# Performance work log

Measured on AMD Instinct MI355X. Metric: run time of the kernel, lower is better.

## Reference

```python
import jax, jax.numpy as jnp
import numpy as np

NUM_HEAD = 8
HIDDEN = 1024


def setup_inputs() -> dict:
    key = jax.random.key(0)
    ks = jax.random.split(key, 7)
    B, Q, K = 2, 256, 256
    return {
        "query": jax.random.normal(ks[0], (B, Q, HIDDEN), jnp.float32),
        "keys": jax.random.normal(ks[1], (B, K, HIDDEN), jnp.float32),
        "values": jax.random.normal(ks[2], (B, K, HIDDEN), jnp.float32),
        "mask": jax.random.randint(ks[3], (B, K), 0, 2, jnp.int32),
        "W_q": jax.random.normal(ks[4], (HIDDEN, HIDDEN), jnp.float32),
        "W_k": jax.random.normal(ks[5], (HIDDEN, HIDDEN), jnp.float32),
        "V_a": jax.random.normal(ks[6], (HIDDEN,), jnp.float32),
    }


def reference(query, keys, values, mask, W_q, W_k, V_a):
    B, Q, H = query.shape
    K = keys.shape[1]
    h_q = query @ W_q                                   # [B,Q,H]
    h_k = keys @ W_k                                    # [B,K,H]
    # additive (Bahdanau) scores, split hidden into heads and sum per head
    h = jnp.tanh(h_q[:, :, None, :] + h_k[:, None, :, :]) * V_a   # [B,Q,K,H]
    logits = h.reshape(B, Q, K, NUM_HEAD, H // NUM_HEAD).sum(-1)  # [B,Q,K,h]
    logits = jnp.transpose(logits, (0, 3, 1, 2))        # [B,h,Q,K]
    penalty = (1.0 - mask.astype(jnp.float32)) * 99.0   # [B,K]
    logits = logits - penalty[:, None, None, :]
    weights = jax.nn.softmax(logits, axis=-1)           # [B,h,Q,K]
    v = values.reshape(B, K, NUM_HEAD, H // NUM_HEAD)   # [B,K,h,d]
    ctx = jnp.einsum('bhqk,bkhd->bqhd', weights, v).reshape(B, Q, H)
    return ctx, weights
```

## Files before the change

### kernel.cpp

```cpp
#include <hip/hip_runtime.h>
#include <hip/hip_bf16.h>


#define TANH_SCALE 2.88539008177792681472f
#define LOG2E      1.44269504088896340736f

typedef __attribute__((ext_vector_type(8))) short bf16x8_t;
typedef __attribute__((ext_vector_type(4))) float f32x4_t;

__device__ inline ushort bf16_rne(float f) {
  unsigned u = __float_as_uint(f);
  u += 0x7FFFu + ((u >> 16) & 1u);
  return (ushort)(u >> 16);
}
__device__ inline float bf16_to_f(ushort h) { return __uint_as_float((unsigned)h << 16); }
__device__ inline void split1(float v, ushort& hi, ushort& lo) {
  hi = bf16_rne(v);
  lo = bf16_rne(v - bf16_to_f(hi));
}

__global__ __launch_bounds__(256) void prep(
    const float* __restrict__ query, const float* __restrict__ keys,
    const float* __restrict__ Wq, const float* __restrict__ Wk,
    ushort* __restrict__ qhi, ushort* __restrict__ qlo,
    ushort* __restrict__ khi, ushort* __restrict__ klo,
    ushort* __restrict__ wqthi, ushort* __restrict__ wqtlo,
    ushort* __restrict__ wkthi, ushort* __restrict__ wktlo)
{
  __shared__ float t[64][65];
  const int bid = blockIdx.x, tid = threadIdx.x;
  if (bid < 1024) {
    const int z = bid >> 9;
    const float* in = z ? keys : query;
    ushort* hi = z ? khi : qhi;
    ushort* lo = z ? klo : qlo;
    const size_t i = ((size_t)(bid & 511) * 256 + tid) * 4;
    float4 v = *(const float4*)(in + i);
    ushort h0, h1, h2, h3, l0, l1, l2, l3;
    split1(v.x, h0, l0); split1(v.y, h1, l1);
    split1(v.z, h2, l2); split1(v.w, h3, l3);
    *(ushort4*)(hi + i) = make_ushort4(h0, h1, h2, h3);
    *(ushort4*)(lo + i) = make_ushort4(l0, l1, l2, l3);
  } else {
    const int idx = bid - 1024;
    const int z = idx >> 8;
    const float* W = z ? Wk : Wq;
    ushort* thi = z ? wkthi : wqthi;
    ushort* tlo = z ? wktlo : wqtlo;
    const int n0 = (idx & 15) * 64, h0 = ((idx >> 4) & 15) * 64;
    const int r = tid >> 4, c = (tid & 15) * 4;
#pragma unroll
    for (int i = 0; i < 4; ++i) {
      const int rr = r + i * 16;
      float4 wv = *(const float4*)(W + (size_t)(h0 + rr) * 1024 + n0 + c);
      t[rr][c + 0] = wv.x; t[rr][c + 1] = wv.y;
      t[rr][c + 2] = wv.z; t[rr][c + 3] = wv.w;
    }
    __syncthreads();
#pragma unroll
    for (int i = 0; i < 4; ++i) {
      const int rr = r + i * 16;
      ushort h0v, h1v, h2v, h3v, l0v, l1v, l2v, l3v;
      split1(t[c + 0][rr] * TANH_SCALE, h0v, l0v);
      split1(t[c + 1][rr] * TANH_SCALE, h1v, l1v);
      split1(t[c + 2][rr] * TANH_SCALE, h2v, l2v);
      split1(t[c + 3][rr] * TANH_SCALE, h3v, l3v);
      *(ushort4*)(thi + (size_t)(n0 + rr) * 1024 + h0 + c) = make_ushort4(h0v, h1v, h2v, h3v);
      *(ushort4*)(tlo + (size_t)(n0 + rr) * 1024 + h0 + c) = make_ushort4(l0v, l1v, l2v, l3v);
    }
  }
}

__global__ __launch_bounds__(256) void gemm_mfma(
    const ushort* __restrict__ qhi, const ushort* __restrict__ qlo,
    const ushort* __restrict__ khi, const ushort* __restrict__ klo,
    const ushort* __restrict__ wqthi, const ushort* __restrict__ wqtlo,
    const ushort* __restrict__ wkthi, const ushort* __restrict__ wktlo,
    float* __restrict__ hq_f, float* __restrict__ hkT)
{
  const int z = blockIdx.y;
  const int bid = blockIdx.x;
  int m0, n0, ldc;
  const ushort *Ah_g, *Al_g, *Bh_g, *Bl_g;
  float* C;
  if (z == 0) {
    m0 = (bid >> 4) * 64; n0 = (bid & 15) * 64; ldc = 1024;
    Ah_g = qhi; Al_g = qlo; Bh_g = wqthi; Bl_g = wqtlo; C = hq_f;
  } else {
    m0 = (bid >> 3) * 64; n0 = (bid & 7) * 64; ldc = 512;
    Ah_g = wkthi; Al_g = wktlo; Bh_g = khi; Bl_g = klo; C = hkT;
  }

  __shared__ __align__(16) ushort Ah[64 * 40];
  __shared__ __align__(16) ushort Al[64 * 40];
  __shared__ __align__(16) ushort Bh[64 * 40];
  __shared__ __align__(16) ushort Bl[64 * 40];

  const int tid = threadIdx.x;
  const int srow = tid >> 2, skc = (tid & 3) * 8;
  const size_t gA = (size_t)(m0 + srow) * 1024 + skc;
  const size_t gB = (size_t)(n0 + srow) * 1024 + skc;
  const int soff = srow * 40 + skc;

  uint4 rah = *(const uint4*)(Ah_g + gA);
  uint4 ral = *(const uint4*)(Al_g + gA);
  uint4 rbh = *(const uint4*)(Bh_g + gB);
  uint4 rbl = *(const uint4*)(Bl_g + gB);

  const int w = __builtin_amdgcn_readfirstlane(tid >> 6);
  const int lane = tid & 63;
  const int wm = (w >> 1) * 32, wn = (w & 1) * 32;
  const int fr = lane & 15, kg = lane >> 4;
  const int aoff = (wm + fr) * 40 + kg * 8;
  const int boff = (wn + fr) * 40 + kg * 8;

  f32x4_t acc[2][2] = {};

  for (int kk = 0; kk < 1024; kk += 32) {
    __syncthreads();
    *(uint4*)(Ah + soff) = rah;
    *(uint4*)(Al + soff) = ral;
    *(uint4*)(Bh + soff) = rbh;
    *(uint4*)(Bl + soff) = rbl;
    __syncthreads();

    if (kk + 32 < 1024) {
      rah = *(const uint4*)(Ah_g + gA + kk + 32);
      ral = *(const uint4*)(Al_g + gA + kk + 32);
      rbh = *(const uint4*)(Bh_g + gB + kk + 32);
      rbl = *(const uint4*)(Bl_g + gB + kk + 32);
    }

    bf16x8_t ah0 = *(const bf16x8_t*)(Ah + aoff);
    bf16x8_t ah1 = *(const bf16x8_t*)(Ah + aoff + 16 * 40);
    bf16x8_t al0 = *(const bf16x8_t*)(Al + aoff);
    bf16x8_t al1 = *(const bf16x8_t*)(Al + aoff + 16 * 40);
    bf16x8_t bh0 = *(const bf16x8_t*)(Bh + boff);
    bf16x8_t bh1 = *(const bf16x8_t*)(Bh + boff + 16 * 40);
    bf16x8_t bl0 = *(const bf16x8_t*)(Bl + boff);
    bf16x8_t bl1 = *(const bf16x8_t*)(Bl + boff + 16 * 40);

    acc[0][0] = __builtin_amdgcn_mfma_f32_16x16x32_bf16(ah0, bh0, acc[0][0], 0, 0, 0);
    acc[0][1] = __builtin_amdgcn_mfma_f32_16x16x32_bf16(ah0, bh1, acc[0][1], 0, 0, 0);
    acc[1][0] = __builtin_amdgcn_mfma_f32_16x16x32_bf16(ah1, bh0, acc[1][0], 0, 0, 0);
    acc[1][1] = __builtin_amdgcn_mfma_f32_16x16x32_bf16(ah1, bh1, acc[1][1], 0, 0, 0);
    acc[0][0] = __builtin_amdgcn_mfma_f32_16x16x32_bf16(ah0, bl0, acc[0][0], 0, 0, 0);
    acc[0][1] = __builtin_amdgcn_mfma_f32_16x16x32_bf16(ah0, bl1, acc[0][1], 0, 0, 0);
    acc[1][0] = __builtin_amdgcn_mfma_f32_16x16x32_bf16(ah1, bl0, acc[1][0], 0, 0, 0);
    acc[1][1] = __builtin_amdgcn_mfma_f32_16x16x32_bf16(ah1, bl1, acc[1][1], 0, 0, 0);
    acc[0][0] = __builtin_amdgcn_mfma_f32_16x16x32_bf16(al0, bh0, acc[0][0], 0, 0, 0);
    acc[0][1] = __builtin_amdgcn_mfma_f32_16x16x32_bf16(al0, bh1, acc[0][1], 0, 0, 0);
    acc[1][0] = __builtin_amdgcn_mfma_f32_16x16x32_bf16(al1, bh0, acc[1][0], 0, 0, 0);
    acc[1][1] = __builtin_amdgcn_mfma_f32_16x16x32_bf16(al1, bh1, acc[1][1], 0, 0, 0);
  }

#pragma unroll
  for (int fm = 0; fm < 2; ++fm)
#pragma unroll
    for (int fn = 0; fn < 2; ++fn) {
      const int col = n0 + wn + fn * 16 + fr;
#pragma unroll
      for (int j = 0; j < 4; ++j) {
        const int row = m0 + wm + fm * 16 + kg * 4 + j;
        C[(size_t)row * ldc + col] = acc[fm][fn][j];
      }
    }
}

__global__ __launch_bounds__(256) void attn_fused(
    const float* __restrict__ hq_f, const float* __restrict__ hkT,
    const float* __restrict__ Va, const int* __restrict__ mask,
    const float* __restrict__ values,
    float* __restrict__ weights, float* __restrict__ ctx)
{
  __shared__ float red_m[4];
  __shared__ float red_s[4];
  __shared__ __align__(16) float w_lds[2][256];
  __shared__ __align__(16) float pv_part[4][32][4];

  const int tid = threadIdx.x;
  const int lane = tid & 63;
  const int w = __builtin_amdgcn_readfirstlane(tid >> 6);
  const int r = w >> 1, kh = w & 1;
  const int bid = blockIdx.x;
  const int bh = bid >> 7;
  const int b = bh & 1, h = bh >> 1;
  const int q = (bid & 127) * 2 + r;
  const int k0 = kh * 128 + 2 * lane;

  const int2 mk = *(const int2*)(mask + b * 256 + k0);
  const float pen0 = 99.0f * (1.0f - (float)mk.x);
  const float pen1 = 99.0f * (1.0f - (float)mk.y);

  float ssum = Va[h * 128 + lane] + Va[h * 128 + 64 + lane];
#pragma unroll
  for (int off = 32; off; off >>= 1) ssum += __shfl_xor(ssum, off, 64);

  const float* ekb = hkT + (size_t)(h * 128) * 512 + b * 256 + k0;
  const float* hqp = hq_f + (size_t)(b * 256 + q) * 1024 + h * 128;
  const float* vap = Va + h * 128;

  float a0e = 0.f, a0o = 0.f, a1e = 0.f, a1o = 0.f;

  float2 e0 = *(const float2*)(ekb + 0 * 512);
  float2 e1 = *(const float2*)(ekb + 1 * 512);
  float2 e2 = *(const float2*)(ekb + 2 * 512);
  float2 e3 = *(const float2*)(ekb + 3 * 512);
  float4 hq4 = *(const float4*)(hqp);
  float4 va4 = *(const float4*)(vap);

  for (int g = 0; g < 32; ++g) {
    float2 n0v, n1v, n2v, n3v; float4 nhq, nva;
    if (g < 31) {
      const float* nb = ekb + (size_t)(4 * g + 4) * 512;
      n0v = *(const float2*)(nb + 0 * 512);
      n1v = *(const float2*)(nb + 1 * 512);
      n2v = *(const float2*)(nb + 2 * 512);
      n3v = *(const float2*)(nb + 3 * 512);
      nhq = *(const float4*)(hqp + 4 * g + 4);
      nva = *(const float4*)(vap + 4 * g + 4);
    }
    {
      float t0 = __builtin_amdgcn_exp2f(hq4.x + e0.x);
      float t1 = __builtin_amdgcn_exp2f(hq4.x + e0.y);
      a0e += va4.x * __builtin_amdgcn_rcpf(t0 + 1.0f);
      a1e += va4.x * __builtin_amdgcn_rcpf(t1 + 1.0f);
      float u0 = __builtin_amdgcn_exp2f(hq4.y + e1.x);
      float u1 = __builtin_amdgcn_exp2f(hq4.y + e1.y);
      a0o += va4.y * __builtin_amdgcn_rcpf(u0 + 1.0f);
      a1o += va4.y * __builtin_amdgcn_rcpf(u1 + 1.0f);
      float v0 = __builtin_amdgcn_exp2f(hq4.z + e2.x);
      float v1 = __builtin_amdgcn_exp2f(hq4.z + e2.y);
      a0e += va4.z * __builtin_amdgcn_rcpf(v0 + 1.0f);
      a1e += va4.z * __builtin_amdgcn_rcpf(v1 + 1.0f);
      float x0 = __builtin_amdgcn_exp2f(hq4.w + e3.x);
      float x1 = __builtin_amdgcn_exp2f(hq4.w + e3.y);
      a0o += va4.w * __builtin_amdgcn_rcpf(x0 + 1.0f);
      a1o += va4.w * __builtin_amdgcn_rcpf(x1 + 1.0f);
    }
    if (g < 31) {
      e0 = n0v; e1 = n1v; e2 = n2v; e3 = n3v;
      hq4 = nhq; va4 = nva;
    }
  }

  const float l0 = ssum - 2.0f * (a0e + a0o) - pen0;
  const float l1 = ssum - 2.0f * (a1e + a1o) - pen1;

  float mx = fmaxf(l0, l1);
#pragma unroll
  for (int off = 32; off; off >>= 1) mx = fmaxf(mx, __shfl_xor(mx, off, 64));
  if (lane == 0) red_m[w] = mx;
  __syncthreads();
  const float m = fmaxf(mx, red_m[w ^ 1]);

  float p0 = __builtin_amdgcn_exp2f((l0 - m) * LOG2E);
  float p1 = __builtin_amdgcn_exp2f((l1 - m) * LOG2E);
  float s = p0 + p1;
#pragma unroll
  for (int off = 32; off; off >>= 1) s += __shfl_xor(s, off, 64);
  if (lane == 0) red_s[w] = s;
  __syncthreads();
  const float invS = 1.0f / (s + red_s[w ^ 1]);
  p0 *= invS; p1 *= invS;

  float* wp = weights + ((size_t)((b * 8 + h) * 256) + q) * 256 + k0;
  wp[0] = p0; wp[1] = p1;
  w_lds[r][k0] = p0; w_lds[r][k0 + 1] = p1;
  __syncthreads();

  const int d4 = lane & 31, ks = lane >> 5;
  const float* vb = values + (size_t)(b * 256 + kh * 128 + ks * 64) * 1024 + h * 128 + d4 * 4;
  const float* wr = &w_lds[r][kh * 128 + ks * 64];
  float4 accE = make_float4(0, 0, 0, 0), accO = make_float4(0, 0, 0, 0);
#pragma unroll 4
  for (int k = 0; k < 64; k += 2) {
    float4 v0 = *(const float4*)&vb[k * 1024];
    float4 v1 = *(const float4*)&vb[(k + 1) * 1024];
    float w0 = wr[k], w1 = wr[k + 1];
    accE.x += w0 * v0.x; accE.y += w0 * v0.y; accE.z += w0 * v0.z; accE.w += w0 * v0.w;
    accO.x += w1 * v1.x; accO.y += w1 * v1.y; accO.z += w1 * v1.z; accO.w += w1 * v1.w;
  }
  float4 a;
  a.x = accE.x + accO.x; a.y = accE.y + accO.y;
  a.z = accE.z + accO.z; a.w = accE.w + accO.w;
  a.x += __shfl_xor(a.x, 32, 64);
  a.y += __shfl_xor(a.y, 32, 64);
  a.z += __shfl_xor(a.z, 32, 64);
  a.w += __shfl_xor(a.w, 32, 64);
  if (lane < 32) *(float4*)&pv_part[w][d4][0] = a;
  __syncthreads();

  if (tid < 64) {
    const int rr = tid >> 5, dd = tid & 31;
    float4 pa = *(const float4*)&pv_part[2 * rr][dd][0];
    float4 pb = *(const float4*)&pv_part[2 * rr + 1][dd][0];
    float4 o;
    o.x = pa.x + pb.x; o.y = pa.y + pb.y; o.z = pa.z + pb.z; o.w = pa.w + pb.w;
    const int qg = (bid & 127) * 2 + rr;
    *(float4*)&ctx[(size_t)(b * 256 + qg) * 1024 + h * 128 + dd * 4] = o;
  }
}

extern "C" void kernel_launch(void* const* d_in, const int* in_sizes, int n_in,
                              void* d_out, int out_size, void* d_ws, size_t ws_size,
                              hipStream_t stream) {
  const float* query  = (const float*)d_in[0];
  const float* keys   = (const float*)d_in[1];
  const float* values = (const float*)d_in[2];
  const int*   mask   = (const int*)d_in[3];
  const float* Wq     = (const float*)d_in[4];
  const float* Wk     = (const float*)d_in[5];
  const float* Va     = (const float*)d_in[6];

  float* ctx     = (float*)d_out;
  float* weights = ctx + 524288;

  ushort* qhi   = (ushort*)d_ws;
  ushort* qlo   = qhi + 524288;
  ushort* khi   = qlo + 524288;
  ushort* klo   = khi + 524288;
  ushort* wqthi = klo + 524288;
  ushort* wqtlo = wqthi + 1048576;
  ushort* wkthi = wqtlo + 1048576;
  ushort* wktlo = wkthi + 1048576;
  float*  hq_f  = (float*)(wktlo + 1048576);
  float*  hkT   = hq_f + 524288;

  prep<<<dim3(1536), 256, 0, stream>>>(query, keys, Wq, Wk,
                                       qhi, qlo, khi, klo,
                                       wqthi, wqtlo, wkthi, wktlo);
  gemm_mfma<<<dim3(128, 2), 256, 0, stream>>>(qhi, qlo, khi, klo,
                                              wqthi, wqtlo, wkthi, wktlo, hq_f, hkT);
  attn_fused<<<dim3(2048), 256, 0, stream>>>(hq_f, hkT, Va, mask, values, weights, ctx);
}
```

Before: 76.60 us.

## Tile attention kernel over 8 queries per block to reuse key projections

The fused attention kernel now handles 8 query rows per block, with one key per thread, instead of 2 queries with 2 keys per thread. Each thread keeps its key-projection and V_a chunk in registers and reuses them across all 8 queries. The PV product also reuses each loaded value row for two queries. The aim is to cut repeated global loads of hkT and values. In exchange the grid is 4x smaller (512 blocks), register pressure rises, and the transcendental work per thread grows 4x.

```diff
diff --git a/kernel.cpp b/kernel.cpp
--- a/kernel.cpp
+++ b/kernel.cpp
@@ -167,138 +167,147 @@
     }
 }
 
+#define TT(hqv, hkv, vav, accq)                                     \
+  {                                                                 \
+    float a_ = (hqv) + (hkv);                                       \
+    float e_ = __builtin_amdgcn_exp2f(a_);                          \
+    accq += (vav) * __builtin_amdgcn_rcpf(e_ + 1.0f);               \
+  }
+
 __global__ __launch_bounds__(256) void attn_fused(
     const float* __restrict__ hq_f, const float* __restrict__ hkT,
     const float* __restrict__ Va, const int* __restrict__ mask,
     const float* __restrict__ values,
     float* __restrict__ weights, float* __restrict__ ctx)
 {
-  __shared__ float red_m[4];
-  __shared__ float red_s[4];
-  __shared__ __align__(16) float w_lds[2][256];
-  __shared__ __align__(16) float pv_part[4][32][4];
+  __shared__ float red_m[4][8];
+  __shared__ float red_s[4][8];
+  __shared__ __align__(16) float P_lds[8][256];
 
   const int tid = threadIdx.x;
   const int lane = tid & 63;
   const int w = __builtin_amdgcn_readfirstlane(tid >> 6);
-  const int r = w >> 1, kh = w & 1;
   const int bid = blockIdx.x;
-  const int bh = bid >> 7;
+  const int bh = bid >> 5;
   const int b = bh & 1, h = bh >> 1;
-  const int q = (bid & 127) * 2 + r;
-  const int k0 = kh * 128 + 2 * lane;
-
-  const int2 mk = *(const int2*)(mask + b * 256 + k0);
-  const float pen0 = 99.0f * (1.0f - (float)mk.x);
-  const float pen1 = 99.0f * (1.0f - (float)mk.y);
+  const int qt = (bid & 31) * 8;
+  const int k = w * 64 + lane;
+
+  const float pen = 99.0f * (1.0f - (float)mask[b * 256 + k]);
 
   float ssum = Va[h * 128 + lane] + Va[h * 128 + 64 + lane];
 #pragma unroll
   for (int off = 32; off; off >>= 1) ssum += __shfl_xor(ssum, off, 64);
 
-  const float* ekb = hkT + (size_t)(h * 128) * 512 + b * 256 + k0;
-  const float* hqp = hq_f + (size_t)(b * 256 + q) * 1024 + h * 128;
+  const float* hkp = hkT + (size_t)(h * 128) * 512 + b * 256 + k;
+  const float* hqb = hq_f + (size_t)(b * 256 + qt) * 1024 + h * 128;
   const float* vap = Va + h * 128;
 
-  float a0e = 0.f, a0o = 0.f, a1e = 0.f, a1o = 0.f;
-
-  float2 e0 = *(const float2*)(ekb + 0 * 512);
-  float2 e1 = *(const float2*)(ekb + 1 * 512);
-  float2 e2 = *(const float2*)(ekb + 2 * 512);
-  float2 e3 = *(const float2*)(ekb + 3 * 512);
-  float4 hq4 = *(const float4*)(hqp);
-  float4 va4 = *(const float4*)(vap);
-
-  for (int g = 0; g < 32; ++g) {
-    float2 n0v, n1v, n2v, n3v; float4 nhq, nva;
-    if (g < 31) {
-      const float* nb = ekb + (size_t)(4 * g + 4) * 512;
-      n0v = *(const float2*)(nb + 0 * 512);
-      n1v = *(const float2*)(nb + 1 * 512);
-      n2v = *(const float2*)(nb + 2 * 512);
-      n3v = *(const float2*)(nb + 3 * 512);
-      nhq = *(const float4*)(hqp + 4 * g + 4);
-      nva = *(const float4*)(vap + 4 * g + 4);
-    }
-    {
-      float t0 = __builtin_amdgcn_exp2f(hq4.x + e0.x);
-      float t1 = __builtin_amdgcn_exp2f(hq4.x + e0.y);
-      a0e += va4.x * __builtin_amdgcn_rcpf(t0 + 1.0f);
-      a1e += va4.x * __builtin_amdgcn_rcpf(t1 + 1.0f);
-      float u0 = __builtin_amdgcn_exp2f(hq4.y + e1.x);
-      float u1 = __builtin_amdgcn_exp2f(hq4.y + e1.y);
-      a0o += va4.y * __builtin_amdgcn_rcpf(u0 + 1.0f);
-      a1o += va4.y * __builtin_amdgcn_rcpf(u1 + 1.0f);
-      float v0 = __builtin_amdgcn_exp2f(hq4.z + e2.x);
-      float v1 = __builtin_amdgcn_exp2f(hq4.z + e2.y);
-      a0e += va4.z * __builtin_amdgcn_rcpf(v0 + 1.0f);
-      a1e += va4.z * __builtin_amdgcn_rcpf(v1 + 1.0f);
-      float x0 = __builtin_amdgcn_exp2f(hq4.w + e3.x);
-      float x1 = __builtin_amdgcn_exp2f(hq4.w + e3.y);
-      a0o += va4.w * __builtin_amdgcn_rcpf(x0 + 1.0f);
-      a1o += va4.w * __builtin_amdgcn_rcpf(x1 + 1.0f);
-    }
-    if (g < 31) {
-      e0 = n0v; e1 = n1v; e2 = n2v; e3 = n3v;
-      hq4 = nhq; va4 = nva;
-    }
-  }
-
-  const float l0 = ssum - 2.0f * (a0e + a0o) - pen0;
-  const float l1 = ssum - 2.0f * (a1e + a1o) - pen1;
-
-  float mx = fmaxf(l0, l1);
-#pragma unroll
-  for (int off = 32; off; off >>= 1) mx = fmaxf(mx, __shfl_xor(mx, off, 64));
-  if (lane == 0) red_m[w] = mx;
+  float acc[8] = {0.f, 0.f, 0.f, 0.f, 0.f, 0.f, 0.f, 0.f};
+
+  float hkc[16], vac[16];
+#pragma unroll
+  for (int j = 0; j < 16; ++j) hkc[j] = hkp[(size_t)j * 512];
+#pragma unroll
+  for (int j = 0; j < 16; ++j) vac[j] = vap[j];
+
+  for (int ch = 0; ch < 8; ++ch) {
+    const int d0 = ch * 16;
+    float hkn[16], van[16];
+    if (ch < 7) {
+#pragma unroll
+      for (int j = 0; j < 16; ++j) hkn[j] = hkp[(size_t)(d0 + 16 + j) * 512];
+#pragma unroll
+      for (int j = 0; j < 16; ++j) van[j] = vap[d0 + 16 + j];
+    }
+#pragma unroll
+    for (int q = 0; q < 8; ++q) {
+      const float* hqq = hqb + (size_t)q * 1024 + d0;
+      float4 a0 = *(const float4*)(hqq + 0);
+      float4 a1 = *(const float4*)(hqq + 4);
+      float4 a2 = *(const float4*)(hqq + 8);
+      float4 a3 = *(const float4*)(hqq + 12);
+      TT(a0.x, hkc[0],  vac[0],  acc[q]);
+      TT(a0.y, hkc[1],  vac[1],  acc[q]);
+      TT(a0.z, hkc[2],  vac[2],  acc[q]);
+      TT(a0.w, hkc[3],  vac[3],  acc[q]);
+      TT(a1.x, hkc[4],  vac[4],  acc[q]);
+      TT(a1.y, hkc[5],  vac[5],  acc[q]);
+      TT(a1.z, hkc[6],  vac[6],  acc[q]);
+      TT(a1.w, hkc[7],  vac[7],  acc[q]);
+      TT(a2.x, hkc[8],  vac[8],  acc[q]);
+      TT(a2.y, hkc[9],  vac[9],  acc[q]);
+      TT(a2.z, hkc[10], vac[10], acc[q]);
+      TT(a2.w, hkc[11], vac[11], acc[q]);
+      TT(a3.x, hkc[12], vac[12], acc[q]);
+      TT(a3.y, hkc[13], vac[13], acc[q]);
+      TT(a3.z, hkc[14], vac[14], acc[q]);
+      TT(a3.w, hkc[15], vac[15], acc[q]);
+    }
+    if (ch < 7) {
+#pragma unroll
+      for (int j = 0; j < 16; ++j) { hkc[j] = hkn[j]; vac[j] = van[j]; }
+    }
+  }
+
+  float l[8], p[8];
+#pragma unroll
+  for (int q = 0; q < 8; ++q) l[q] = ssum - 2.0f * acc[q] - pen;
+
+#pragma unroll
+  for (int q = 0; q < 8; ++q) {
+    float m = l[q];
+#pragma unroll
+    for (int off = 32; off; off >>= 1) m = fmaxf(m, __shfl_xor(m, off, 64));
+    if (lane == 0) red_m[w][q] = m;
+  }
   __syncthreads();
-  const float m = fmaxf(mx, red_m[w ^ 1]);
-
-  float p0 = __builtin_amdgcn_exp2f((l0 - m) * LOG2E);
-  float p1 = __builtin_amdgcn_exp2f((l1 - m) * LOG2E);
-  float s = p0 + p1;
-#pragma unroll
-  for (int off = 32; off; off >>= 1) s += __shfl_xor(s, off, 64);
-  if (lane == 0) red_s[w] = s;
+#pragma unroll
+  for (int q = 0; q < 8; ++q) {
+    float m = fmaxf(fmaxf(red_m[0][q], red_m[1][q]), fmaxf(red_m[2][q], red_m[3][q]));
+    p[q] = __builtin_amdgcn_exp2f((l[q] - m) * LOG2E);
+  }
+#pragma unroll
+  for (int q = 0; q < 8; ++q) {
+    float s = p[q];
+#pragma unroll
+    for (int off = 32; off; off >>= 1) s += __shfl_xor(s, off, 64);
+    if (lane == 0) red_s[w][q] = s;
+  }
   __syncthreads();
-  const float invS = 1.0f / (s + red_s[w ^ 1]);
-  p0 *= invS; p1 *= invS;
-
-  float* wp = weights + ((size_t)((b * 8 + h) * 256) + q) * 256 + k0;
-  wp[0] = p0; wp[1] = p1;
-  w_lds[r][k0] = p0; w_lds[r][k0 + 1] = p1;
+#pragma unroll
+  for (int q = 0; q < 8; ++q) {
+    const float s = (red_s[0][q] + red_s[1][q]) + (red_s[2][q] + red_s[3][q]);
+    const float pq = p[q] / s;
+    weights[((size_t)((b * 8 + h) * 256) + qt + q) * 256 + k] = pq;
+    P_lds[q][k] = pq;
+  }
   __syncthreads();
 
   const int d4 = lane & 31, ks = lane >> 5;
-  const float* vb = values + (size_t)(b * 256 + kh * 128 + ks * 64) * 1024 + h * 128 + d4 * 4;
-  const float* wr = &w_lds[r][kh * 128 + ks * 64];
-  float4 accE = make_float4(0, 0, 0, 0), accO = make_float4(0, 0, 0, 0);
-#pragma unroll 4
-  for (int k = 0; k < 64; k += 2) {
-    float4 v0 = *(const float4*)&vb[k * 1024];
-    float4 v1 = *(const float4*)&vb[(k + 1) * 1024];
-    float w0 = wr[k], w1 = wr[k + 1];
-    accE.x += w0 * v0.x; accE.y += w0 * v0.y; accE.z += w0 * v0.z; accE.w += w0 * v0.w;
-    accO.x += w1 * v1.x; accO.y += w1 * v1.y; accO.z += w1 * v1.z; accO.w += w1 * v1.w;
-  }
-  float4 a;
-  a.x = accE.x + accO.x; a.y = accE.y + accO.y;
-  a.z = accE.z + accO.z; a.w = accE.w + accO.w;
-  a.x += __shfl_xor(a.x, 32, 64);
-  a.y += __shfl_xor(a.y, 32, 64);
-  a.z += __shfl_xor(a.z, 32, 64);
-  a.w += __shfl_xor(a.w, 32, 64);
-  if (lane < 32) *(float4*)&pv_part[w][d4][0] = a;
-  __syncthreads();
-
-  if (tid < 64) {
-    const int rr = tid >> 5, dd = tid & 31;
-    float4 pa = *(const float4*)&pv_part[2 * rr][dd][0];
-    float4 pb = *(const float4*)&pv_part[2 * rr + 1][dd][0];
-    float4 o;
-    o.x = pa.x + pb.x; o.y = pa.y + pb.y; o.z = pa.z + pb.z; o.w = pa.w + pb.w;
-    const int qg = (bid & 127) * 2 + rr;
-    *(float4*)&ctx[(size_t)(b * 256 + qg) * 1024 + h * 128 + dd * 4] = o;
+  const int q0 = w * 2, q1 = q0 + 1;
+  const float* vb = values + (size_t)(b * 256 + ks * 128) * 1024 + h * 128 + d4 * 4;
+  float4 A0 = make_float4(0, 0, 0, 0), A1 = make_float4(0, 0, 0, 0);
+#pragma unroll 2
+  for (int k4 = 0; k4 < 32; ++k4) {
+    float4 p0v = *(const float4*)&P_lds[q0][ks * 128 + k4 * 4];
+    float4 p1v = *(const float4*)&P_lds[q1][ks * 128 + k4 * 4];
+#pragma unroll
+    for (int j = 0; j < 4; ++j) {
+      float4 v = *(const float4*)(vb + (size_t)(k4 * 4 + j) * 1024);
+      const float pj0 = (j == 0) ? p0v.x : (j == 1) ? p0v.y : (j == 2) ? p0v.z : p0v.w;
+      const float pj1 = (j == 0) ? p1v.x : (j == 1) ? p1v.y : (j == 2) ? p1v.z : p1v.w;
+      A0.x += pj0 * v.x; A0.y += pj0 * v.y; A0.z += pj0 * v.z; A0.w += pj0 * v.w;
+      A1.x += pj1 * v.x; A1.y += pj1 * v.y; A1.z += pj1 * v.z; A1.w += pj1 * v.w;
+    }
+  }
+  A0.x += __shfl_xor(A0.x, 32, 64); A0.y += __shfl_xor(A0.y, 32, 64);
+  A0.z += __shfl_xor(A0.z, 32, 64); A0.w += __shfl_xor(A0.w, 32, 64);
+  A1.x += __shfl_xor(A1.x, 32, 64); A1.y += __shfl_xor(A1.y, 32, 64);
+  A1.z += __shfl_xor(A1.z, 32, 64); A1.w += __shfl_xor(A1.w, 32, 64);
+  if (lane < 32) {
+    *(float4*)&ctx[(size_t)(b * 256 + qt + q0) * 1024 + h * 128 + d4 * 4] = A0;
+    *(float4*)&ctx[(size_t)(b * 256 + qt + q1) * 1024 + h * 128 + d4 * 4] = A1;
   }
 }
 
@@ -332,5 +341,5 @@
                                        wqthi, wqtlo, wkthi, wktlo);
   gemm_mfma<<<dim3(128, 2), 256, 0, stream>>>(qhi, qlo, khi, klo,
                                               wqthi, wqtlo, wkthi, wktlo, hq_f, hkT);
-  attn_fused<<<dim3(2048), 256, 0, stream>>>(hq_f, hkT, Va, mask, values, weights, ctx);
-}
+  attn_fused<<<dim3(512), 256, 0, stream>>>(hq_f, hkT, Va, mask, values, weights, ctx);
+}
```

Result: no change. 75.49 us (-1.5%).
